# Optimization experiments

Measured on AMD Instinct MI355X. Metric: run time of the kernel, lower is better.

Reference implementation:

```python
import jax, jax.numpy as jnp
import numpy as np

B, N, C, H = 8, 4096, 768, 8


def setup_inputs() -> dict:
    key = jax.random.key(0)
    k1, k2, k3 = jax.random.split(key, 3)
    x = jax.random.normal(k1, (B, N, C), dtype=jnp.float32)
    W_qkv = jax.random.normal(k2, (C, 3 * C), dtype=jnp.float32) * 0.02
    W_proj = jax.random.normal(k3, (C, C), dtype=jnp.float32) * 0.02
    b_proj = jnp.zeros((C,), dtype=jnp.float32)
    temp = jnp.ones((H, 1, 1), dtype=jnp.float32)
    return {"x": x, "W_qkv": W_qkv, "W_proj": W_proj, "b_proj": b_proj, "temp": temp}


def reference(x, W_qkv, W_proj, b_proj, temp):
    b, n, c = x.shape
    h = temp.shape[0]
    d = c // h
    # qkv: [B,N,3C] -> [B,N,H,D,3]  (matches tf.reshape split order)
    qkv = (x @ W_qkv).reshape(b, n, h, d, 3)
    q, k, v = qkv[..., 0], qkv[..., 1], qkv[..., 2]
    # L2-normalize along the patch axis (axis=1), as tf.linalg.normalize
    q = q / jnp.linalg.norm(q, axis=1, keepdims=True)
    k = k / jnp.linalg.norm(k, axis=1, keepdims=True)
    # channel-wise (cross-covariance) attention: [B,H,D,D]
    attn = jnp.einsum('bnhd,bnhe->bhde', q, k) * temp
    attn = jax.nn.softmax(attn, axis=-1)
    # apply to v and fold heads back: [B,N,C]
    y = jnp.einsum('bhde,bnhe->bnhd', attn, v).reshape(b, n, c)
    return y @ W_proj + b_proj
```

## Files before the change

### kernel.cpp

```cpp
#include <hip/hip_runtime.h>

typedef __attribute__((ext_vector_type(8))) short short8;
typedef __attribute__((ext_vector_type(4))) float f32x4;

__device__ inline unsigned short f2b(float f) {
  unsigned int u = __builtin_bit_cast(unsigned int, f);
  u = (u + 0x7FFFu + ((u >> 16) & 1u)) >> 16;
  return (unsigned short)u;
}
__device__ inline float b2f(unsigned short s) {
  unsigned int u = ((unsigned int)s) << 16;
  return __builtin_bit_cast(float, u);
}

__device__ inline void async16(const void* g, void* l) {
  __builtin_amdgcn_global_load_lds((__attribute__((address_space(1))) void*)(g),
                                   (__attribute__((address_space(3))) void*)(l), 16, 0, 0);
}

__global__ void cvt_x(const float4* __restrict__ x, ushort4* __restrict__ xb, int n4) {
  int i = blockIdx.x * blockDim.x + threadIdx.x;
  int stride = gridDim.x * blockDim.x;
  for (; i < n4; i += stride) {
    float4 v = x[i];
    ushort4 o;
    o.x = f2b(v.x); o.y = f2b(v.y); o.z = f2b(v.z); o.w = f2b(v.w);
    xb[i] = o;
  }
}

__global__ __launch_bounds__(256) void t_wqkv(const float* __restrict__ W, unsigned short* __restrict__ Wt) {
  __shared__ float tile[32][33];
  int j0 = blockIdx.x * 32, c0 = blockIdx.y * 32;
  int tx = threadIdx.x & 31, ty = threadIdx.x >> 5;
#pragma unroll
  for (int r = 0; r < 32; r += 8)
    tile[ty + r][tx] = W[(size_t)(c0 + ty + r) * 2304 + j0 + tx];
  __syncthreads();
#pragma unroll
  for (int r = 0; r < 32; r += 8) {
    int j = j0 + ty + r;
    int h = j / 288, rem = j - h * 288;
    int d = rem / 3, s = rem - d * 3;
    int jj = s * 768 + h * 96 + d;
    Wt[(size_t)jj * 768 + c0 + tx] = f2b(tile[tx][ty + r]);
  }
}

__global__ __launch_bounds__(256) void t_wproj(const float* __restrict__ W, unsigned short* __restrict__ Wt) {
  __shared__ float tile[32][33];
  int j0 = blockIdx.x * 32, c0 = blockIdx.y * 32;
  int tx = threadIdx.x & 31, ty = threadIdx.x >> 5;
#pragma unroll
  for (int r = 0; r < 32; r += 8)
    tile[ty + r][tx] = W[(size_t)(c0 + ty + r) * 768 + j0 + tx];
  __syncthreads();
#pragma unroll
  for (int r = 0; r < 32; r += 8)
    Wt[(size_t)(j0 + ty + r) * 768 + c0 + tx] = f2b(tile[tx][ty + r]);
}

__global__ __launch_bounds__(256) void gemm_qkv(
    const unsigned short* __restrict__ A, const unsigned short* __restrict__ Bt,
    unsigned short* __restrict__ Q, unsigned short* __restrict__ Kd, unsigned short* __restrict__ V) {
  __shared__ __align__(16) unsigned short As[128 * 64];
  __shared__ __align__(16) unsigned short Bs[128 * 64];
  const int tid = threadIdx.x;
  const int wave = tid >> 6, lane = tid & 63;
  const int mlane = lane & 15, quad = lane >> 4;
  const int m0 = blockIdx.x * 128, n0 = blockIdx.y * 128;
  const int wm = (wave >> 1) * 64, wn = (wave & 1) * 64;
  f32x4 acc[4][4] = {};
  for (int k0 = 0; k0 < 768; k0 += 64) {
    __syncthreads();
#pragma unroll
    for (int t = 0; t < 4; ++t) {
      int ebase = t * 256 + (wave << 6);
      int e = ebase + lane;
      int row = e >> 3, c8 = e & 7;
      async16(A + (size_t)(m0 + row) * 768 + k0 + c8 * 8, As + ebase * 8);
      async16(Bt + (size_t)(n0 + row) * 768 + k0 + c8 * 8, Bs + ebase * 8);
    }
    __syncthreads();
#pragma unroll
    for (int kk = 0; kk < 64; kk += 32) {
      short8 a[4], b[4];
#pragma unroll
      for (int f = 0; f < 4; ++f)
        a[f] = *(const short8*)&As[(wm + f * 16 + mlane) * 64 + kk + quad * 8];
#pragma unroll
      for (int f = 0; f < 4; ++f)
        b[f] = *(const short8*)&Bs[(wn + f * 16 + mlane) * 64 + kk + quad * 8];
#pragma unroll
      for (int i = 0; i < 4; ++i)
#pragma unroll
        for (int j = 0; j < 4; ++j)
          acc[i][j] = __builtin_amdgcn_mfma_f32_16x16x32_bf16(a[i], b[j], acc[i][j], 0, 0, 0);
    }
  }
  const int bb = m0 >> 12;
  const int nb = (m0 & 4095) + wm + quad * 4;
#pragma unroll
  for (int fn = 0; fn < 4; ++fn) {
    int jj = n0 + wn + fn * 16 + mlane;
    int s = jj / 768;
    int hd = jj - s * 768;
    int h = hd / 96;
    int d = hd - h * 96;
    unsigned short* dst = (s == 0) ? Q : (s == 1) ? Kd : V;
    size_t colbase = ((size_t)(bb * 8 + h) * 4096) * 96 + d;
#pragma unroll
    for (int fm = 0; fm < 4; ++fm) {
      int n = nb + fm * 16;
#pragma unroll
      for (int r = 0; r < 4; ++r)
        dst[colbase + (size_t)(n + r) * 96] = f2b(acc[fm][fn][r]);
    }
  }
}

__global__ __launch_bounds__(256) void sumsq_qk(
    const unsigned short* __restrict__ Q, const unsigned short* __restrict__ Kd,
    float* __restrict__ sq, float* __restrict__ sk) {
  int bh = blockIdx.x, chunk = blockIdx.y;
  int t = threadIdx.x;
  __shared__ float lq[96], lk[96];
  if (t < 96) { lq[t] = 0.f; lk[t] = 0.f; }
  __syncthreads();
  int c = t % 48, rg = t / 48;
  if (rg < 5) {
    const unsigned int* qp = (const unsigned int*)(Q + (size_t)bh * 4096 * 96);
    const unsigned int* kp = (const unsigned int*)(Kd + (size_t)bh * 4096 * 96);
    int base = chunk * 256;
    float aq0 = 0, aq1 = 0, ak0 = 0, ak1 = 0;
    for (int n = rg; n < 256; n += 5) {
      unsigned int qv = qp[(size_t)(base + n) * 48 + c];
      unsigned int kv = kp[(size_t)(base + n) * 48 + c];
      float q0 = b2f(qv & 0xffff), q1 = b2f(qv >> 16);
      float k0 = b2f(kv & 0xffff), k1 = b2f(kv >> 16);
      aq0 += q0 * q0; aq1 += q1 * q1; ak0 += k0 * k0; ak1 += k1 * k1;
    }
    atomicAdd(&lq[2 * c], aq0); atomicAdd(&lq[2 * c + 1], aq1);
    atomicAdd(&lk[2 * c], ak0); atomicAdd(&lk[2 * c + 1], ak1);
  }
  __syncthreads();
  if (t < 96) {
    atomicAdd(&sq[bh * 96 + t], lq[t]);
    atomicAdd(&sk[bh * 96 + t], lk[t]);
  }
}

__global__ __launch_bounds__(256) void attn_partial(
    const unsigned short* __restrict__ Q, const unsigned short* __restrict__ Kd,
    float* __restrict__ Spart) {
  int chunk = blockIdx.x;
  int bh = blockIdx.y;
  __shared__ __align__(16) unsigned short QT[96 * 72];
  __shared__ __align__(16) unsigned short KT[96 * 72];
  int t = threadIdx.x;
  int wave = t >> 6, lane = t & 63, mlane = lane & 15, quad = lane >> 4;
  int wrow = (wave >> 1) * 48, wcol = (wave & 1) * 48;
  f32x4 acc[3][3] = {};
  const unsigned int* qp = (const unsigned int*)(Q + (size_t)bh * 4096 * 96);
  const unsigned int* kp = (const unsigned int*)(Kd + (size_t)bh * 4096 * 96);
  int c = t % 48, rg = t / 48;
  int nbeg = chunk * 256;
  for (int n0 = nbeg; n0 < nbeg + 256; n0 += 64) {
    __syncthreads();
    if (rg < 5) {
      for (int n = rg; n < 64; n += 5) {
        unsigned int qv = qp[(size_t)(n0 + n) * 48 + c];
        unsigned int kv = kp[(size_t)(n0 + n) * 48 + c];
        QT[(2 * c) * 72 + n] = (unsigned short)(qv & 0xffff);
        QT[(2 * c + 1) * 72 + n] = (unsigned short)(qv >> 16);
        KT[(2 * c) * 72 + n] = (unsigned short)(kv & 0xffff);
        KT[(2 * c + 1) * 72 + n] = (unsigned short)(kv >> 16);
      }
    }
    __syncthreads();
#pragma unroll
    for (int kk = 0; kk < 64; kk += 32) {
      short8 a[3], b[3];
#pragma unroll
      for (int f = 0; f < 3; ++f)
        a[f] = *(const short8*)&QT[(wrow + f * 16 + mlane) * 72 + kk + quad * 8];
#pragma unroll
      for (int f = 0; f < 3; ++f)
        b[f] = *(const short8*)&KT[(wcol + f * 16 + mlane) * 72 + kk + quad * 8];
#pragma unroll
      for (int i = 0; i < 3; ++i)
#pragma unroll
        for (int j = 0; j < 3; ++j)
          acc[i][j] = __builtin_amdgcn_mfma_f32_16x16x32_bf16(a[i], b[j], acc[i][j], 0, 0, 0);
    }
  }
  float* dst = Spart + ((size_t)bh * 16 + chunk) * 9216;
#pragma unroll
  for (int i = 0; i < 3; ++i)
#pragma unroll
    for (int j = 0; j < 3; ++j)
#pragma unroll
      for (int r = 0; r < 4; ++r)
        dst[(wrow + i * 16 + quad * 4 + r) * 96 + wcol + j * 16 + mlane] = acc[i][j][r];
}

__global__ __launch_bounds__(256) void attn_finalize(
    const float* __restrict__ Spart, const float* __restrict__ sq,
    const float* __restrict__ sk, const float* __restrict__ temp,
    unsigned short* __restrict__ P) {
  int bh = blockIdx.x, h = bh & 7;
  __shared__ float S[9216];
  __shared__ float rk[96];
  int t = threadIdx.x;
  const float* base = Spart + (size_t)bh * 16 * 9216;
  for (int i = t; i < 9216; i += 256) {
    float s = 0.f;
#pragma unroll
    for (int c2 = 0; c2 < 16; ++c2) s += base[(size_t)c2 * 9216 + i];
    S[i] = s;
  }
  if (t < 96) rk[t] = rsqrtf(sk[bh * 96 + t]);
  __syncthreads();
  if (t < 96) {
    int d = t;
    float rq = rsqrtf(sq[bh * 96 + d]);
    float tm = temp[h];
    float mx = -1e30f;
    for (int e = 0; e < 96; ++e) {
      float v = S[d * 96 + e] * rq * rk[e] * tm;
      S[d * 96 + e] = v;
      mx = fmaxf(mx, v);
    }
    float sum = 0.f;
    for (int e = 0; e < 96; ++e) {
      float v = expf(S[d * 96 + e] - mx);
      S[d * 96 + e] = v;
      sum += v;
    }
    float inv = 1.0f / sum;
    for (int e = 0; e < 96; ++e)
      P[(size_t)bh * 9216 + d * 96 + e] = f2b(S[d * 96 + e] * inv);
  }
}

__global__ __launch_bounds__(256) void gemm_pv(
    const unsigned short* __restrict__ V, const unsigned short* __restrict__ P,
    unsigned short* __restrict__ y) {
  int bh = blockIdx.y;
  int b = bh >> 3, h = bh & 7;
  int m0 = blockIdx.x * 128;
  int t = threadIdx.x, wave = t >> 6, lane = t & 63, mlane = lane & 15, quad = lane >> 4;
  const unsigned short* Vb = V + (size_t)bh * 4096 * 96;
  const unsigned short* Pb = P + (size_t)bh * 9216;
  f32x4 acc[2][6] = {};
#pragma unroll
  for (int kk = 0; kk < 96; kk += 32) {
    short8 a[2], bfr[6];
#pragma unroll
    for (int i = 0; i < 2; ++i)
      a[i] = *(const short8*)&Vb[(size_t)(m0 + wave * 32 + i * 16 + mlane) * 96 + kk + quad * 8];
#pragma unroll
    for (int j = 0; j < 6; ++j)
      bfr[j] = *(const short8*)&Pb[(j * 16 + mlane) * 96 + kk + quad * 8];
#pragma unroll
    for (int i = 0; i < 2; ++i)
#pragma unroll
      for (int j = 0; j < 6; ++j)
        acc[i][j] = __builtin_amdgcn_mfma_f32_16x16x32_bf16(a[i], bfr[j], acc[i][j], 0, 0, 0);
  }
#pragma unroll
  for (int i = 0; i < 2; ++i) {
    int n = m0 + wave * 32 + i * 16 + quad * 4;
#pragma unroll
    for (int j = 0; j < 6; ++j) {
      int d = j * 16 + mlane;
#pragma unroll
      for (int r = 0; r < 4; ++r)
        y[((size_t)b * 4096 + n + r) * 768 + h * 96 + d] = f2b(acc[i][j][r]);
    }
  }
}

__global__ __launch_bounds__(256) void gemm_proj(
    const unsigned short* __restrict__ A, const unsigned short* __restrict__ Bt,
    const float* __restrict__ bias, float* __restrict__ out) {
  __shared__ __align__(16) unsigned short As[128 * 64];
  __shared__ __align__(16) unsigned short Bs[128 * 64];
  const int tid = threadIdx.x;
  const int wave = tid >> 6, lane = tid & 63;
  const int mlane = lane & 15, quad = lane >> 4;
  const int m0 = blockIdx.x * 128, n0 = blockIdx.y * 128;
  const int wm = (wave >> 1) * 64, wn = (wave & 1) * 64;
  f32x4 acc[4][4] = {};
  for (int k0 = 0; k0 < 768; k0 += 64) {
    __syncthreads();
#pragma unroll
    for (int t = 0; t < 4; ++t) {
      int ebase = t * 256 + (wave << 6);
      int e = ebase + lane;
      int row = e >> 3, c8 = e & 7;
      async16(A + (size_t)(m0 + row) * 768 + k0 + c8 * 8, As + ebase * 8);
      async16(Bt + (size_t)(n0 + row) * 768 + k0 + c8 * 8, Bs + ebase * 8);
    }
    __syncthreads();
#pragma unroll
    for (int kk = 0; kk < 64; kk += 32) {
      short8 a[4], b[4];
#pragma unroll
      for (int f = 0; f < 4; ++f)
        a[f] = *(const short8*)&As[(wm + f * 16 + mlane) * 64 + kk + quad * 8];
#pragma unroll
      for (int f = 0; f < 4; ++f)
        b[f] = *(const short8*)&Bs[(wn + f * 16 + mlane) * 64 + kk + quad * 8];
#pragma unroll
      for (int i = 0; i < 4; ++i)
#pragma unroll
        for (int j = 0; j < 4; ++j)
          acc[i][j] = __builtin_amdgcn_mfma_f32_16x16x32_bf16(a[i], b[j], acc[i][j], 0, 0, 0);
    }
  }
#pragma unroll
  for (int fn = 0; fn < 4; ++fn) {
    int col = n0 + wn + fn * 16 + mlane;
    float bv = bias[col];
#pragma unroll
    for (int fm = 0; fm < 4; ++fm) {
      int m = m0 + wm + fm * 16 + quad * 4;
#pragma unroll
      for (int r = 0; r < 4; ++r)
        out[(size_t)(m + r) * 768 + col] = acc[fm][fn][r] + bv;
    }
  }
}

extern "C" void kernel_launch(void* const* d_in, const int* in_sizes, int n_in,
                              void* d_out, int out_size, void* d_ws, size_t ws_size,
                              hipStream_t stream) {
  const float* x = (const float*)d_in[0];
  const float* Wqkv = (const float*)d_in[1];
  const float* Wproj = (const float*)d_in[2];
  const float* bias = (const float*)d_in[3];
  const float* temp = (const float*)d_in[4];
  float* out = (float*)d_out;

  char* ws = (char*)d_ws;
  size_t off = 0;
  auto alloc = [&](size_t bytes) -> void* {
    void* p = ws + off;
    off += (bytes + 255) & ~(size_t)255;
    return p;
  };
  unsigned short* xb = (unsigned short*)alloc(32768ull * 768 * 2);
  unsigned short* Wtq = (unsigned short*)alloc(2304ull * 768 * 2);
  unsigned short* Wtp = (unsigned short*)alloc(768ull * 768 * 2);
  unsigned short* Q = (unsigned short*)alloc(64ull * 4096 * 96 * 2);
  unsigned short* Kd = (unsigned short*)alloc(64ull * 4096 * 96 * 2);
  unsigned short* V = (unsigned short*)alloc(64ull * 4096 * 96 * 2);
  float* sq = (float*)alloc(64 * 96 * 4);
  float* sk = (float*)alloc(64 * 96 * 4);
  unsigned short* P = (unsigned short*)alloc(64ull * 9216 * 2);
  (void)off; (void)ws_size; (void)in_sizes; (void)n_in; (void)out_size;

  float* Spart = out;

  cvt_x<<<4096, 256, 0, stream>>>((const float4*)x, (ushort4*)xb, 32768 * 768 / 4);
  t_wqkv<<<dim3(72, 24), 256, 0, stream>>>(Wqkv, Wtq);
  t_wproj<<<dim3(24, 24), 256, 0, stream>>>(Wproj, Wtp);
  gemm_qkv<<<dim3(256, 18), 256, 0, stream>>>(xb, Wtq, Q, Kd, V);
  hipMemsetAsync(sq, 0, 64 * 96 * 4, stream);
  hipMemsetAsync(sk, 0, 64 * 96 * 4, stream);
  sumsq_qk<<<dim3(64, 16), 256, 0, stream>>>(Q, Kd, sq, sk);
  attn_partial<<<dim3(16, 64), 256, 0, stream>>>(Q, Kd, Spart);
  attn_finalize<<<64, 256, 0, stream>>>(Spart, sq, sk, temp, P);
  gemm_pv<<<dim3(32, 64), 256, 0, stream>>>(V, P, xb );
  gemm_proj<<<dim3(256, 6), 256, 0, stream>>>(xb , Wtp, bias, out);
}
```

Baseline: 550.4 us.

## Swizzle GEMM LDS tiles, stage QKV epilogue through LDS, fuse sum-of-squares

Applies an XOR swizzle to the LDS layout of the A/B tiles in both the QKV and projection GEMMs to cut bank conflicts on the MFMA fragment reads. The QKV epilogue now stages the bf16 tile in LDS and writes 16-byte vectors per row, replacing scattered 2-byte stores. It also computes the Q/K squared-norm partials from those values and accumulates them with atomics, which removes the separate sumsq_qk kernel and its re-read of Q and K. The cost is an extra LDS round trip and barriers in the epilogue, plus more global atomics per block.

```diff
diff --git a/kernel.cpp b/kernel.cpp
--- a/kernel.cpp
+++ b/kernel.cpp
@@ -62,9 +62,11 @@
 
 __global__ __launch_bounds__(256) void gemm_qkv(
     const unsigned short* __restrict__ A, const unsigned short* __restrict__ Bt,
-    unsigned short* __restrict__ Q, unsigned short* __restrict__ Kd, unsigned short* __restrict__ V) {
-  __shared__ __align__(16) unsigned short As[128 * 64];
-  __shared__ __align__(16) unsigned short Bs[128 * 64];
+    unsigned short* __restrict__ Q, unsigned short* __restrict__ Kd, unsigned short* __restrict__ V,
+    float* __restrict__ sq, float* __restrict__ sk) {
+  __shared__ __align__(16) unsigned short smem[2 * 128 * 64];
+  unsigned short* As = smem;
+  unsigned short* Bs = smem + 128 * 64;
   const int tid = threadIdx.x;
   const int wave = tid >> 6, lane = tid & 63;
   const int mlane = lane & 15, quad = lane >> 4;
@@ -77,20 +79,25 @@
     for (int t = 0; t < 4; ++t) {
       int ebase = t * 256 + (wave << 6);
       int e = ebase + lane;
-      int row = e >> 3, c8 = e & 7;
-      async16(A + (size_t)(m0 + row) * 768 + k0 + c8 * 8, As + ebase * 8);
-      async16(Bt + (size_t)(n0 + row) * 768 + k0 + c8 * 8, Bs + ebase * 8);
+      int row = e >> 3;
+      int g = (e & 7) ^ (row & 7);
+      async16(A + (size_t)(m0 + row) * 768 + k0 + g * 8, As + ebase * 8);
+      async16(Bt + (size_t)(n0 + row) * 768 + k0 + g * 8, Bs + ebase * 8);
     }
     __syncthreads();
 #pragma unroll
     for (int kk = 0; kk < 64; kk += 32) {
       short8 a[4], b[4];
 #pragma unroll
-      for (int f = 0; f < 4; ++f)
-        a[f] = *(const short8*)&As[(wm + f * 16 + mlane) * 64 + kk + quad * 8];
-#pragma unroll
-      for (int f = 0; f < 4; ++f)
-        b[f] = *(const short8*)&Bs[(wn + f * 16 + mlane) * 64 + kk + quad * 8];
+      for (int f = 0; f < 4; ++f) {
+        int ra = wm + f * 16 + mlane;
+        a[f] = *(const short8*)&As[ra * 64 + ((((kk >> 3) + quad) ^ (ra & 7)) << 3)];
+      }
+#pragma unroll
+      for (int f = 0; f < 4; ++f) {
+        int rb = wn + f * 16 + mlane;
+        b[f] = *(const short8*)&Bs[rb * 64 + ((((kk >> 3) + quad) ^ (rb & 7)) << 3)];
+      }
 #pragma unroll
       for (int i = 0; i < 4; ++i)
 #pragma unroll
@@ -98,55 +105,59 @@
           acc[i][j] = __builtin_amdgcn_mfma_f32_16x16x32_bf16(a[i], b[j], acc[i][j], 0, 0, 0);
     }
   }
+  __syncthreads();
+  unsigned short* Cs = smem;
+#pragma unroll
+  for (int i = 0; i < 4; ++i)
+#pragma unroll
+    for (int j = 0; j < 4; ++j)
+#pragma unroll
+      for (int r = 0; r < 4; ++r) {
+        int row = wm + i * 16 + quad * 4 + r;
+        int col = wn + j * 16 + mlane;
+        int pc = (col >> 3) ^ (((row >> 2) & 3) << 1);
+        Cs[row * 128 + pc * 8 + (col & 7)] = f2b(acc[i][j][r]);
+      }
+  __syncthreads();
+  const int s = n0 / 768;
+  unsigned short* dst = (s == 0) ? Q : (s == 1) ? Kd : V;
   const int bb = m0 >> 12;
-  const int nb = (m0 & 4095) + wm + quad * 4;
-#pragma unroll
-  for (int fn = 0; fn < 4; ++fn) {
-    int jj = n0 + wn + fn * 16 + mlane;
-    int s = jj / 768;
-    int hd = jj - s * 768;
-    int h = hd / 96;
-    int d = hd - h * 96;
-    unsigned short* dst = (s == 0) ? Q : (s == 1) ? Kd : V;
-    size_t colbase = ((size_t)(bb * 8 + h) * 4096) * 96 + d;
-#pragma unroll
-    for (int fm = 0; fm < 4; ++fm) {
-      int n = nb + fm * 16;
-#pragma unroll
-      for (int r = 0; r < 4; ++r)
-        dst[colbase + (size_t)(n + r) * 96] = f2b(acc[fm][fn][r]);
-    }
-  }
-}
-
-__global__ __launch_bounds__(256) void sumsq_qk(
-    const unsigned short* __restrict__ Q, const unsigned short* __restrict__ Kd,
-    float* __restrict__ sq, float* __restrict__ sk) {
-  int bh = blockIdx.x, chunk = blockIdx.y;
-  int t = threadIdx.x;
-  __shared__ float lq[96], lk[96];
-  if (t < 96) { lq[t] = 0.f; lk[t] = 0.f; }
-  __syncthreads();
-  int c = t % 48, rg = t / 48;
-  if (rg < 5) {
-    const unsigned int* qp = (const unsigned int*)(Q + (size_t)bh * 4096 * 96);
-    const unsigned int* kp = (const unsigned int*)(Kd + (size_t)bh * 4096 * 96);
-    int base = chunk * 256;
-    float aq0 = 0, aq1 = 0, ak0 = 0, ak1 = 0;
-    for (int n = rg; n < 256; n += 5) {
-      unsigned int qv = qp[(size_t)(base + n) * 48 + c];
-      unsigned int kv = kp[(size_t)(base + n) * 48 + c];
-      float q0 = b2f(qv & 0xffff), q1 = b2f(qv >> 16);
-      float k0 = b2f(kv & 0xffff), k1 = b2f(kv >> 16);
-      aq0 += q0 * q0; aq1 += q1 * q1; ak0 += k0 * k0; ak1 += k1 * k1;
-    }
-    atomicAdd(&lq[2 * c], aq0); atomicAdd(&lq[2 * c + 1], aq1);
-    atomicAdd(&lk[2 * c], ak0); atomicAdd(&lk[2 * c + 1], ak1);
-  }
-  __syncthreads();
-  if (t < 96) {
-    atomicAdd(&sq[bh * 96 + t], lq[t]);
-    atomicAdd(&sk[bh * 96 + t], lk[t]);
+  const int c = tid & 15;
+  float ss[8] = {0.f, 0.f, 0.f, 0.f, 0.f, 0.f, 0.f, 0.f};
+  int jj = n0 + c * 8;
+  int hd = jj - s * 768;
+  int h = hd / 96, d = hd - h * 96;
+  size_t rowbase = ((size_t)(bb * 8 + h) * 4096 + (m0 & 4095)) * 96 + d;
+#pragma unroll
+  for (int p = 0; p < 8; ++p) {
+    int row = p * 16 + (tid >> 4);
+    int pcc = c ^ (((row >> 2) & 3) << 1);
+    short8 val = *(const short8*)&Cs[row * 128 + pcc * 8];
+    *(short8*)&dst[rowbase + (size_t)row * 96] = val;
+    if (s < 2) {
+#pragma unroll
+      for (int e = 0; e < 8; ++e) {
+        float f = b2f((unsigned short)val[e]);
+        ss[e] += f * f;
+      }
+    }
+  }
+  if (s < 2) {
+#pragma unroll
+    for (int e = 0; e < 8; ++e) {
+      ss[e] += __shfl_xor(ss[e], 16);
+      ss[e] += __shfl_xor(ss[e], 32);
+    }
+    if (mlane == lane) {
+      float* gdst = (s == 0) ? sq : sk;
+#pragma unroll
+      for (int e = 0; e < 8; ++e) {
+        int jje = n0 + lane * 8 + e;
+        int hde = jje - s * 768;
+        int he = hde / 96, de = hde - he * 96;
+        atomicAdd(&gdst[(bb * 8 + he) * 96 + de], ss[e]);
+      }
+    }
   }
 }
 
@@ -284,8 +295,9 @@
 __global__ __launch_bounds__(256) void gemm_proj(
     const unsigned short* __restrict__ A, const unsigned short* __restrict__ Bt,
     const float* __restrict__ bias, float* __restrict__ out) {
-  __shared__ __align__(16) unsigned short As[128 * 64];
-  __shared__ __align__(16) unsigned short Bs[128 * 64];
+  __shared__ __align__(16) unsigned short smem[2 * 128 * 64];
+  unsigned short* As = smem;
+  unsigned short* Bs = smem + 128 * 64;
   const int tid = threadIdx.x;
   const int wave = tid >> 6, lane = tid & 63;
   const int mlane = lane & 15, quad = lane >> 4;
@@ -298,20 +310,25 @@
     for (int t = 0; t < 4; ++t) {
       int ebase = t * 256 + (wave << 6);
       int e = ebase + lane;
-      int row = e >> 3, c8 = e & 7;
-      async16(A + (size_t)(m0 + row) * 768 + k0 + c8 * 8, As + ebase * 8);
-      async16(Bt + (size_t)(n0 + row) * 768 + k0 + c8 * 8, Bs + ebase * 8);
+      int row = e >> 3;
+      int g = (e & 7) ^ (row & 7);
+      async16(A + (size_t)(m0 + row) * 768 + k0 + g * 8, As + ebase * 8);
+      async16(Bt + (size_t)(n0 + row) * 768 + k0 + g * 8, Bs + ebase * 8);
     }
     __syncthreads();
 #pragma unroll
     for (int kk = 0; kk < 64; kk += 32) {
       short8 a[4], b[4];
 #pragma unroll
-      for (int f = 0; f < 4; ++f)
-        a[f] = *(const short8*)&As[(wm + f * 16 + mlane) * 64 + kk + quad * 8];
-#pragma unroll
-      for (int f = 0; f < 4; ++f)
-        b[f] = *(const short8*)&Bs[(wn + f * 16 + mlane) * 64 + kk + quad * 8];
+      for (int f = 0; f < 4; ++f) {
+        int ra = wm + f * 16 + mlane;
+        a[f] = *(const short8*)&As[ra * 64 + ((((kk >> 3) + quad) ^ (ra & 7)) << 3)];
+      }
+#pragma unroll
+      for (int f = 0; f < 4; ++f) {
+        int rb = wn + f * 16 + mlane;
+        b[f] = *(const short8*)&Bs[rb * 64 + ((((kk >> 3) + quad) ^ (rb & 7)) << 3)];
+      }
 #pragma unroll
       for (int i = 0; i < 4; ++i)
 #pragma unroll
@@ -366,10 +383,9 @@
   cvt_x<<<4096, 256, 0, stream>>>((const float4*)x, (ushort4*)xb, 32768 * 768 / 4);
   t_wqkv<<<dim3(72, 24), 256, 0, stream>>>(Wqkv, Wtq);
   t_wproj<<<dim3(24, 24), 256, 0, stream>>>(Wproj, Wtp);
-  gemm_qkv<<<dim3(256, 18), 256, 0, stream>>>(xb, Wtq, Q, Kd, V);
   hipMemsetAsync(sq, 0, 64 * 96 * 4, stream);
   hipMemsetAsync(sk, 0, 64 * 96 * 4, stream);
-  sumsq_qk<<<dim3(64, 16), 256, 0, stream>>>(Q, Kd, sq, sk);
+  gemm_qkv<<<dim3(256, 18), 256, 0, stream>>>(xb, Wtq, Q, Kd, V, sq, sk);
   attn_partial<<<dim3(16, 64), 256, 0, stream>>>(Q, Kd, Spart);
   attn_finalize<<<64, 256, 0, stream>>>(Spart, sq, sk, temp, P);
   gemm_pv<<<dim3(32, 64), 256, 0, stream>>>(V, P, xb );
```

Measured after the change: 641.5 us. 1.17x slower.
